# Optimization experiments

Measured on AMD Instinct MI355X. Metric: run time of the kernel, lower is better.

## Reference

```python
import jax, jax.numpy as jnp
from jax import lax
import numpy as np

D = 8        # domain_num
L = 12       # label_num
C = 9        # attr_num
W = 128      # window_size
B = 4096
EPS = 1e-5


def setup_inputs() -> dict:
    key = jax.random.key(0)
    ks = jax.random.split(key, 12)
    s = 0.05
    return {
        "x": jax.random.normal(ks[0], (B, C, 1, W), dtype=jnp.float32),
        "weights": jax.random.uniform(ks[1], (B, D), dtype=jnp.float32),
        # per-domain stacked parameters (leading dim D)
        "gamma": jnp.ones((D, C), dtype=jnp.float32),
        "beta": jnp.zeros((D, C), dtype=jnp.float32),
        "w1": jax.random.normal(ks[2], (D, 32, C, 9), dtype=jnp.float32) * s,
        "b1": jax.random.normal(ks[3], (D, 32), dtype=jnp.float32) * s,
        "w2": jax.random.normal(ks[4], (D, 64, 32, 9), dtype=jnp.float32) * s,
        "b2": jax.random.normal(ks[5], (D, 64), dtype=jnp.float32) * s,
        "fcw": jax.random.normal(ks[6], (D, L, 64 * 26), dtype=jnp.float32) * s,
        "fcb": jax.random.normal(ks[7], (D, L), dtype=jnp.float32) * s,
    }


def _maxpool2(h):
    # MaxPool along width, kernel 2 stride 2 (height is 1 and already squeezed)
    b, c, w = h.shape
    return h.reshape(b, c, w // 2, 2).max(axis=-1)


def _branch(x3, gamma, beta, w1, b1, w2, b2, fcw, fcb):
    # x3: [B, C, W]. BatchNorm2d in training mode: batch stats over (N, H, W).
    mean = x3.mean(axis=(0, 2), keepdims=True)
    var = x3.var(axis=(0, 2), keepdims=True)
    xn = (x3 - mean) * lax.rsqrt(var + EPS) * gamma[None, :, None] + beta[None, :, None]
    dn = ('NCH', 'OIH', 'NCH')
    h = lax.conv_general_dilated(xn, w1, (1,), 'VALID', dimension_numbers=dn)
    h = _maxpool2(jax.nn.relu(h + b1[None, :, None]))          # [B,32,60]
    h = lax.conv_general_dilated(h, w2, (1,), 'VALID', dimension_numbers=dn)
    h = _maxpool2(jax.nn.relu(h + b2[None, :, None]))          # [B,64,26]
    flat = h.reshape(h.shape[0], 64 * 26)
    return jax.nn.relu(flat @ fcw.T + fcb)                      # [B,L]


def reference(x, weights, gamma, beta, w1, b1, w2, b2, fcw, fcb):
    x3 = x[:, :, 0, :]  # squeeze height=1 -> [B,C,W]
    per_domain = jax.vmap(_branch, in_axes=(None, 0, 0, 0, 0, 0, 0, 0, 0))(
        x3, gamma, beta, w1, b1, w2, b2, fcw, fcb)              # [D,B,L]
    # vectorized form of the nested python-loop weighted sum over domains
    return jnp.einsum('bd,dbl->bl', weights, per_domain)        # [B,L]
```

## Files before the change

### kernel.cpp

```cpp
#include <hip/hip_runtime.h>
#include <hip/hip_bf16.h>

#define D 8
#define L 12
#define C 9
#define W 128
#define B 4096
#define EPS 1e-5f

typedef __attribute__((ext_vector_type(8))) short v8s;
typedef __attribute__((ext_vector_type(4))) float v4f;

#define OFF_STATS 0
#define OFF_B1E   18432
#define OFF_W1T   18688
#define OFF_W2T   39168
#define OFF_FCWP  112896

#define REGION 2336
#define STRIP  1152

__device__ inline unsigned short f2bf(float f) {
    unsigned u = __builtin_bit_cast(unsigned, f);
    u += 0x7FFFu + ((u >> 16) & 1u);
    return (unsigned short)(u >> 16);
}
__device__ inline unsigned pk2(float a, float b) {
    float2 f2; f2.x = a; f2.y = b;
    __hip_bfloat162 h = __float22bfloat162_rn(f2);
    unsigned u; __builtin_memcpy(&u, &h, 4);
    return u;
}

__global__ void stats_repack_kernel(const float* __restrict__ x,
                                    const float* __restrict__ w2,
                                    const float* __restrict__ fcw,
                                    float* __restrict__ ws,
                                    float* __restrict__ out) {
    const int t = threadIdx.x;
    __shared__ float red2[4][18];
    if (blockIdx.x < 1024) {
        const int rb = blockIdx.x * 4;
        const int w = t & 127, half = t >> 7;
        float s[9], s2[9];
        #pragma unroll
        for (int c = 0; c < 9; c++) { s[c] = 0.f; s2[c] = 0.f; }
        #pragma unroll
        for (int pass = 0; pass < 2; pass++) {
            const int row = rb + pass * 2 + half;
            const float* xr = x + (size_t)row * 1152 + w;
            #pragma unroll
            for (int c = 0; c < 9; c++) {
                float v = xr[c * 128];
                s[c] += v; s2[c] += v * v;
            }
        }
        #pragma unroll
        for (int c = 0; c < 9; c++) {
            #pragma unroll
            for (int off = 32; off >= 1; off >>= 1) {
                s[c]  += __shfl_down(s[c], off);
                s2[c] += __shfl_down(s2[c], off);
            }
        }
        if ((t & 63) == 0) {
            #pragma unroll
            for (int c = 0; c < 9; c++) {
                red2[t >> 6][c] = s[c]; red2[t >> 6][9 + c] = s2[c];
            }
        }
        __syncthreads();
        if (t < 18)
            ws[OFF_STATS + t * 1024 + blockIdx.x] =
                red2[0][t] + red2[1][t] + red2[2][t] + red2[3][t];
    } else if (blockIdx.x < 1152) {
        const int g = (blockIdx.x - 1024) * 4 + (t >> 6);
        const int lane = t & 63;
        const int d = g >> 6, o = g & 63;
        const float* src = w2 + (size_t)(d * 64 + o) * 288;
        short* dst = (short*)(ws + OFF_W2T) + (size_t)d * 18432 + o * 288;
        for (int i = lane; i < 288; i += 64) {
            int ic = i / 9, tap = i % 9;
            dst[tap * 32 + ic] = (short)f2bf(src[i]);
        }
    } else if (blockIdx.x < 1200) {
        const int g = (blockIdx.x - 1152) * 4 + (t >> 6);
        const int lane = t & 63;
        const int dl = g >> 1, half = g & 1;
        const float* src = fcw + (size_t)dl * 1664;
        short* dst = (short*)(ws + OFF_FCWP) + (size_t)dl * 1664;
        for (int i = half * 832 + lane; i < half * 832 + 832; i += 64) {
            int o = i / 26, p = i % 26;
            dst[p * 64 + o] = (short)f2bf(src[i]);
        }
    } else {
        const int base = (blockIdx.x - 1200) * 6144;
        float4 z; z.x = z.y = z.z = z.w = 0.f;
        float4* o4 = (float4*)(out + base);
        for (int i = t; i < 1536; i += 256) o4[i] = z;
    }
}

__global__ void fold1_kernel(const float* __restrict__ w1, const float* __restrict__ b1,
                             const float* __restrict__ gamma, const float* __restrict__ beta,
                             float* __restrict__ ws) {
    const int d = blockIdx.x, t = threadIdx.x;
    const int lane = t & 63, wvq = t >> 6;
    __shared__ float g[9], bt[9];
    for (int c = wvq; c < 9; c += 4) {
        float s = 0.f, s2 = 0.f;
        #pragma unroll
        for (int j = 0; j < 16; j++) {
            s  += ws[OFF_STATS + c * 1024 + lane + 64 * j];
            s2 += ws[OFF_STATS + (9 + c) * 1024 + lane + 64 * j];
        }
        #pragma unroll
        for (int off = 32; off >= 1; off >>= 1) {
            s  += __shfl_down(s, off);
            s2 += __shfl_down(s2, off);
        }
        if (lane == 0) {
            const float N = (float)B * (float)W;
            float m  = s / N;
            float vv = s2 / N - m * m;
            float inv = rsqrtf(vv + EPS);
            float gg = gamma[d * 9 + c] * inv;
            g[c] = gg; bt[c] = beta[d * 9 + c] - gg * m;
        }
    }
    __syncthreads();
    const int o = t >> 3, sub = t & 7;
    short* w1t = (short*)(ws + OFF_W1T);
    short* dst = w1t + (size_t)d * 3072 + o * 96;
    const float* src = w1 + ((size_t)(d * 32 + o)) * 81;
    for (int k = sub * 12; k < sub * 12 + 12; k++) {
        int tap, ch;
        if (k < 64)      { tap = (k >> 5) * 4 + ((k >> 3) & 3); ch = k & 7; }
        else {
            int q = (k >> 3) & 3, j = k & 7;
            if (q == 0)              { tap = 8; ch = j; }
            else if (q == 2)         { tap = j; ch = 8; }
            else if (q == 3 && j==0) { tap = 8; ch = 8; }
            else                     { tap = -1; ch = 0; }
        }
        float v = (tap >= 0) ? src[ch * 9 + tap] * g[ch] : 0.f;
        dst[k] = (short)f2bf(v);
    }
    float bias_part = 0.f;
    for (int tap = sub; tap < 9; tap += 8) {
        for (int c = 0; c < 9; c++)
            bias_part += src[c * 9 + tap] * bt[c];
    }
    bias_part += __shfl_xor(bias_part, 1);
    bias_part += __shfl_xor(bias_part, 2);
    bias_part += __shfl_xor(bias_part, 4);
    if (sub == 0) ws[OFF_B1E + d * 32 + o] = b1[d * 32 + o] + bias_part;
}

__global__ __launch_bounds__(256, 4)
void branch_kernel(const float* __restrict__ x,
                   const float* __restrict__ b2g,
                   const float* __restrict__ fcb,
                   const float* __restrict__ wts,
                   const float* __restrict__ ws,
                   float* __restrict__ out) {
    const int t = threadIdx.x;
    const int lane = t & 63;
    const int wv = t >> 6;
    const int d = blockIdx.y;
    const int b0 = blockIdx.x * 4;
    const short* w1t  = (const short*)(ws + OFF_W1T) + (size_t)d * 3072;
    const short* w2t  = (const short*)(ws + OFF_W2T) + (size_t)d * 18432;
    const short* fcwp = (const short*)(ws + OFF_FCWP) + (size_t)d * 12 * 1664;
    const float* b1e  = ws + OFF_B1E + d * 32;

    __shared__ __align__(16) short lds[4 * REGION];
    short* myr = &lds[wv * REGION];

    const int n = lane & 15, quad = lane >> 4;

    {
        const float* xrow = x + (size_t)(b0 + wv) * 1152;
        unsigned short c8s[2];
        #pragma unroll
        for (int rep = 0; rep < 2; rep++) {
            const int w = lane + rep * 64;
            float v[9];
            #pragma unroll
            for (int c = 0; c < 9; c++) v[c] = xrow[c * 128 + w];
            uint4 lo;
            lo.x = pk2(v[0], v[1]); lo.y = pk2(v[2], v[3]);
            lo.z = pk2(v[4], v[5]); lo.w = pk2(v[6], v[7]);
            *(uint4*)&myr[w * 8] = lo;
            c8s[rep] = f2bf(v[8]);
        }
        {
            uint4 z; z.x = z.y = z.z = z.w = 0;
            if (lane < 16) *(uint4*)&myr[(128 + lane) * 8] = z;
            if (lane < 24) *(uint4*)&myr[STRIP + (120 + lane) * 8] = z;
        }
        #pragma unroll
        for (int rep = 0; rep < 2; rep++) {
            const int w = lane + rep * 64;
            const short c8 = (short)c8s[rep];
            #pragma unroll
            for (int j = 0; j < 8; j++) {
                if (rep == 1 || lane >= j)
                    myr[STRIP + (w - j) * 8 + j] = c8;
            }
        }
    }

    {
        const float bias0 = b1e[n], bias1 = b1e[16 + n];
        v4f acc[8][2];
        #pragma unroll
        for (int mt = 0; mt < 8; mt++)
            #pragma unroll
            for (int nt = 0; nt < 2; nt++) { v4f z = {0.f,0.f,0.f,0.f}; acc[mt][nt] = z; }
        #pragma unroll
        for (int ck = 0; ck < 3; ck++) {
            v8s Bw0 = *(const v8s*)&w1t[n * 96 + ck * 32 + quad * 8];
            v8s Bw1 = *(const v8s*)&w1t[(16 + n) * 96 + ck * 32 + quad * 8];
            #pragma unroll
            for (int mt = 0; mt < 8; mt++) {
                const int rowm = mt * 16 + n;
                int aoff;
                if (ck < 2) aoff = (rowm + ck * 4 + quad) * 8;
                else        aoff = (quad < 2) ? (rowm + 8) * 8
                                              : (STRIP + (rowm + (quad - 2) * 8) * 8);
                v8s Af = *(const v8s*)&myr[aoff];
                acc[mt][0] = __builtin_amdgcn_mfma_f32_16x16x32_bf16(Af, Bw0, acc[mt][0], 0, 0, 0);
                acc[mt][1] = __builtin_amdgcn_mfma_f32_16x16x32_bf16(Af, Bw1, acc[mt][1], 0, 0, 0);
            }
        }
        unsigned held[16];
        #pragma unroll
        for (int mt = 0; mt < 8; mt++)
            #pragma unroll
            for (int nt = 0; nt < 2; nt++) {
                const float bb = nt ? bias1 : bias0;
                float h0  = fmaxf(fmaxf(acc[mt][nt][0], acc[mt][nt][1]) + bb, 0.f);
                float h1v = fmaxf(fmaxf(acc[mt][nt][2], acc[mt][nt][3]) + bb, 0.f);
                held[mt * 2 + nt] = pk2(h0, h1v);
            }
        #pragma unroll
        for (int mt = 0; mt < 8; mt++) {
            const int p = mt * 8 + quad * 2;
            #pragma unroll
            for (int nt = 0; nt < 2; nt++) {
                const unsigned pr = held[mt * 2 + nt];
                const int plane = nt * 2 + (n >> 3);
                const int col = n & 7;
                if (p < 60)     myr[(plane * 73 + p) * 8 + col]     = (short)(pr & 0xFFFFu);
                if (p + 1 < 60) myr[(plane * 73 + p + 1) * 8 + col] = (short)(pr >> 16);
            }
        }
    }

    {
        float biasv[4];
        #pragma unroll
        for (int nt = 0; nt < 4; nt++) biasv[nt] = b2g[d * 64 + nt * 16 + n];
        v4f acc[4][4];
        #pragma unroll
        for (int mt = 0; mt < 4; mt++)
            #pragma unroll
            for (int nt = 0; nt < 4; nt++) { v4f z = {0.f,0.f,0.f,0.f}; acc[mt][nt] = z; }
        for (int tap = 0; tap < 9; tap++) {
            v8s Bw[4];
            #pragma unroll
            for (int nt = 0; nt < 4; nt++)
                Bw[nt] = *(const v8s*)&w2t[(nt * 16 + n) * 288 + tap * 32 + quad * 8];
            #pragma unroll
            for (int mt = 0; mt < 4; mt++) {
                const int row = mt * 16 + n + tap;
                v8s Af = *(const v8s*)&myr[(quad * 73 + row) * 8];
                #pragma unroll
                for (int nt = 0; nt < 4; nt++)
                    acc[mt][nt] = __builtin_amdgcn_mfma_f32_16x16x32_bf16(Af, Bw[nt], acc[mt][nt], 0, 0, 0);
            }
        }
        unsigned held[16];
        #pragma unroll
        for (int mt = 0; mt < 4; mt++)
            #pragma unroll
            for (int nt = 0; nt < 4; nt++) {
                float h0  = fmaxf(fmaxf(acc[mt][nt][0], acc[mt][nt][1]) + biasv[nt], 0.f);
                float h1v = fmaxf(fmaxf(acc[mt][nt][2], acc[mt][nt][3]) + biasv[nt], 0.f);
                held[mt * 4 + nt] = pk2(h0, h1v);
            }
        #pragma unroll
        for (int mt = 0; mt < 4; mt++) {
            const int p = mt * 8 + quad * 2;
            #pragma unroll
            for (int nt = 0; nt < 4; nt++) {
                const unsigned pr = held[mt * 4 + nt];
                const int oc = nt * 16 + n;
                if (p < 26) {
                    const int gs = (oc >> 3) ^ (p & 7);
                    myr[p * 64 + gs * 8 + (oc & 7)] = (short)(pr & 0xFFFFu);
                }
                if (p + 1 < 26) {
                    const int gs = (oc >> 3) ^ ((p + 1) & 7);
                    myr[(p + 1) * 64 + gs * 8 + (oc & 7)] = (short)(pr >> 16);
                }
            }
        }
    }
    __syncthreads();

    {
        const int lrow = (n < 12) ? n : 0;
        v4f acc = {0.f, 0.f, 0.f, 0.f};
        for (int ks = wv; ks < 52; ks += 4) {
            const int p = ks >> 1;
            const int gs = ((ks & 1) * 4 + quad) ^ (p & 7);
            v8s A  = *(const v8s*)&fcwp[lrow * 1664 + ks * 32 + quad * 8];
            v8s Bf = *(const v8s*)&lds[(n & 3) * REGION + p * 64 + gs * 8];
            acc = __builtin_amdgcn_mfma_f32_16x16x32_bf16(A, Bf, acc, 0, 0, 0);
        }
        float* red = (float*)(myr + 1672);
        *(float4*)&red[lane * 4] = *(float4*)&acc;
    }
    __syncthreads();
    if (t < 64) {
        float sum[4] = {0.f, 0.f, 0.f, 0.f};
        #pragma unroll
        for (int w = 0; w < 4; w++) {
            const float* redw = (const float*)(&lds[w * REGION + 1672]);
            float4 v = *(const float4*)&redw[lane * 4];
            sum[0] += v.x; sum[1] += v.y; sum[2] += v.z; sum[3] += v.w;
        }
        if (n < 4) {
            const float wgt = wts[(size_t)(b0 + n) * 8 + d];
            #pragma unroll
            for (int r = 0; r < 4; r++) {
                const int l = quad * 4 + r;
                if (l < 12) {
                    float v = fmaxf(sum[r] + fcb[d * 12 + l], 0.f);
                    atomicAdd(&out[(size_t)(b0 + n) * 12 + l], wgt * v);
                }
            }
        }
    }
}

extern "C" void kernel_launch(void* const* d_in, const int* in_sizes, int n_in,
                              void* d_out, int out_size, void* d_ws, size_t ws_size,
                              hipStream_t stream) {
    const float* x       = (const float*)d_in[0];
    const float* weights = (const float*)d_in[1];
    const float* gamma   = (const float*)d_in[2];
    const float* beta    = (const float*)d_in[3];
    const float* w1      = (const float*)d_in[4];
    const float* b1      = (const float*)d_in[5];
    const float* w2      = (const float*)d_in[6];
    const float* b2      = (const float*)d_in[7];
    const float* fcw     = (const float*)d_in[8];
    const float* fcb     = (const float*)d_in[9];
    float* ws  = (float*)d_ws;
    float* out = (float*)d_out;

    stats_repack_kernel<<<dim3(1208), 256, 0, stream>>>(x, w2, fcw, ws, out);
    fold1_kernel<<<dim3(D), 256, 0, stream>>>(w1, b1, gamma, beta, ws);
    branch_kernel<<<dim3(B / 4, D), 256, 0, stream>>>(x, b2, fcb, weights, ws, out);
}
```

Before: 223.0 us.

## Fold BN weight folding into stats kernel via last-block atomic; shuffle-build channel-8 strip

Removes the separate fold1 kernel launch. The last stats block, identified by an atomic counter reset with a memset, reduces the statistics and writes the folded conv1 weights and bias for all domains. It also replaces the scattered per-element LDS stores that build the shifted channel-8 strip with wave shuffles and two vectorized 16-byte stores per lane. The trade is an extra memset and a serialized tail in one block that loops over all eight domains, in exchange for one fewer kernel launch.

```diff
diff --git a/kernel.cpp b/kernel.cpp
--- a/kernel.cpp
+++ b/kernel.cpp
@@ -16,6 +16,7 @@
 #define OFF_W1T   18688
 #define OFF_W2T   39168
 #define OFF_FCWP  112896
+#define OFF_CTR   192768
 
 #define REGION 2336
 #define STRIP  1152
@@ -35,10 +36,16 @@
 __global__ void stats_repack_kernel(const float* __restrict__ x,
                                     const float* __restrict__ w2,
                                     const float* __restrict__ fcw,
+                                    const float* __restrict__ gamma,
+                                    const float* __restrict__ beta,
+                                    const float* __restrict__ w1,
+                                    const float* __restrict__ b1,
                                     float* __restrict__ ws,
                                     float* __restrict__ out) {
     const int t = threadIdx.x;
     __shared__ float red2[4][18];
+    __shared__ float gI[9], gM[9], gld[9], btd[9];
+    __shared__ int isLast;
     if (blockIdx.x < 1024) {
         const int rb = blockIdx.x * 4;
         const int w = t & 127, half = t >> 7;
@@ -73,6 +80,70 @@
         if (t < 18)
             ws[OFF_STATS + t * 1024 + blockIdx.x] =
                 red2[0][t] + red2[1][t] + red2[2][t] + red2[3][t];
+        __threadfence();
+        __syncthreads();
+        if (t == 0) {
+            int old = atomicAdd((int*)(ws + OFF_CTR), 1);
+            isLast = (old == 1023);
+        }
+        __syncthreads();
+        if (isLast) {
+            __threadfence();
+            const int lane = t & 63, wv = t >> 6;
+            for (int c = wv; c < 9; c += 4) {
+                float rs = 0.f, rs2 = 0.f;
+                #pragma unroll
+                for (int j = 0; j < 16; j++) {
+                    rs  += ws[OFF_STATS + c * 1024 + lane + 64 * j];
+                    rs2 += ws[OFF_STATS + (9 + c) * 1024 + lane + 64 * j];
+                }
+                #pragma unroll
+                for (int off = 32; off >= 1; off >>= 1) {
+                    rs  += __shfl_down(rs, off);
+                    rs2 += __shfl_down(rs2, off);
+                }
+                if (lane == 0) {
+                    const float N = (float)B * (float)W;
+                    float m  = rs / N;
+                    float vv = rs2 / N - m * m;
+                    gI[c] = rsqrtf(vv + EPS); gM[c] = m;
+                }
+            }
+            __syncthreads();
+            const int o = t >> 3, sub = t & 7;
+            for (int d = 0; d < 8; d++) {
+                if (t < 9) {
+                    float gg = gamma[d * 9 + t] * gI[t];
+                    gld[t] = gg; btd[t] = beta[d * 9 + t] - gg * gM[t];
+                }
+                __syncthreads();
+                short* dst = (short*)(ws + OFF_W1T) + (size_t)d * 3072 + o * 96;
+                const float* src = w1 + ((size_t)(d * 32 + o)) * 81;
+                for (int k = sub * 12; k < sub * 12 + 12; k++) {
+                    int tap, ch;
+                    if (k < 64)      { tap = (k >> 5) * 4 + ((k >> 3) & 3); ch = k & 7; }
+                    else {
+                        int q = (k >> 3) & 3, j = k & 7;
+                        if (q == 0)               { tap = 8; ch = j; }
+                        else if (q == 2)          { tap = j; ch = 8; }
+                        else if (q == 3 && j==0)  { tap = 8; ch = 8; }
+                        else                      { tap = -1; ch = 0; }
+                    }
+                    float v = (tap >= 0) ? src[ch * 9 + tap] * gld[ch] : 0.f;
+                    dst[k] = (short)f2bf(v);
+                }
+                float bias_part = 0.f;
+                for (int tap = sub; tap < 9; tap += 8) {
+                    for (int c2 = 0; c2 < 9; c2++)
+                        bias_part += src[c2 * 9 + tap] * btd[c2];
+                }
+                bias_part += __shfl_xor(bias_part, 1);
+                bias_part += __shfl_xor(bias_part, 2);
+                bias_part += __shfl_xor(bias_part, 4);
+                if (sub == 0) ws[OFF_B1E + d * 32 + o] = b1[d * 32 + o] + bias_part;
+                __syncthreads();
+            }
+        }
     } else if (blockIdx.x < 1152) {
         const int g = (blockIdx.x - 1024) * 4 + (t >> 6);
         const int lane = t & 63;
@@ -99,62 +170,6 @@
         float4* o4 = (float4*)(out + base);
         for (int i = t; i < 1536; i += 256) o4[i] = z;
     }
-}
-
-__global__ void fold1_kernel(const float* __restrict__ w1, const float* __restrict__ b1,
-                             const float* __restrict__ gamma, const float* __restrict__ beta,
-                             float* __restrict__ ws) {
-    const int d = blockIdx.x, t = threadIdx.x;
-    const int lane = t & 63, wvq = t >> 6;
-    __shared__ float g[9], bt[9];
-    for (int c = wvq; c < 9; c += 4) {
-        float s = 0.f, s2 = 0.f;
-        #pragma unroll
-        for (int j = 0; j < 16; j++) {
-            s  += ws[OFF_STATS + c * 1024 + lane + 64 * j];
-            s2 += ws[OFF_STATS + (9 + c) * 1024 + lane + 64 * j];
-        }
-        #pragma unroll
-        for (int off = 32; off >= 1; off >>= 1) {
-            s  += __shfl_down(s, off);
-            s2 += __shfl_down(s2, off);
-        }
-        if (lane == 0) {
-            const float N = (float)B * (float)W;
-            float m  = s / N;
-            float vv = s2 / N - m * m;
-            float inv = rsqrtf(vv + EPS);
-            float gg = gamma[d * 9 + c] * inv;
-            g[c] = gg; bt[c] = beta[d * 9 + c] - gg * m;
-        }
-    }
-    __syncthreads();
-    const int o = t >> 3, sub = t & 7;
-    short* w1t = (short*)(ws + OFF_W1T);
-    short* dst = w1t + (size_t)d * 3072 + o * 96;
-    const float* src = w1 + ((size_t)(d * 32 + o)) * 81;
-    for (int k = sub * 12; k < sub * 12 + 12; k++) {
-        int tap, ch;
-        if (k < 64)      { tap = (k >> 5) * 4 + ((k >> 3) & 3); ch = k & 7; }
-        else {
-            int q = (k >> 3) & 3, j = k & 7;
-            if (q == 0)              { tap = 8; ch = j; }
-            else if (q == 2)         { tap = j; ch = 8; }
-            else if (q == 3 && j==0) { tap = 8; ch = 8; }
-            else                     { tap = -1; ch = 0; }
-        }
-        float v = (tap >= 0) ? src[ch * 9 + tap] * g[ch] : 0.f;
-        dst[k] = (short)f2bf(v);
-    }
-    float bias_part = 0.f;
-    for (int tap = sub; tap < 9; tap += 8) {
-        for (int c = 0; c < 9; c++)
-            bias_part += src[c * 9 + tap] * bt[c];
-    }
-    bias_part += __shfl_xor(bias_part, 1);
-    bias_part += __shfl_xor(bias_part, 2);
-    bias_part += __shfl_xor(bias_part, 4);
-    if (sub == 0) ws[OFF_B1E + d * 32 + o] = b1[d * 32 + o] + bias_part;
 }
 
 __global__ __launch_bounds__(256, 4)
@@ -181,7 +196,7 @@
 
     {
         const float* xrow = x + (size_t)(b0 + wv) * 1152;
-        unsigned short c8s[2];
+        int c8a = 0, c8b = 0;
         #pragma unroll
         for (int rep = 0; rep < 2; rep++) {
             const int w = lane + rep * 64;
@@ -192,23 +207,34 @@
             lo.x = pk2(v[0], v[1]); lo.y = pk2(v[2], v[3]);
             lo.z = pk2(v[4], v[5]); lo.w = pk2(v[6], v[7]);
             *(uint4*)&myr[w * 8] = lo;
-            c8s[rep] = f2bf(v[8]);
-        }
-        {
+            if (rep == 0) c8a = (int)f2bf(v[8]); else c8b = (int)f2bf(v[8]);
+        }
+        if (lane < 16) {
             uint4 z; z.x = z.y = z.z = z.w = 0;
-            if (lane < 16) *(uint4*)&myr[(128 + lane) * 8] = z;
-            if (lane < 24) *(uint4*)&myr[STRIP + (120 + lane) * 8] = z;
-        }
-        #pragma unroll
-        for (int rep = 0; rep < 2; rep++) {
-            const int w = lane + rep * 64;
-            const short c8 = (short)c8s[rep];
-            #pragma unroll
-            for (int j = 0; j < 8; j++) {
-                if (rep == 1 || lane >= j)
-                    myr[STRIP + (w - j) * 8 + j] = c8;
-            }
-        }
+            *(uint4*)&myr[(128 + lane) * 8] = z;
+            *(uint4*)&myr[STRIP + (128 + lane) * 8] = z;
+        }
+        unsigned short r0[8], r1[8];
+        r0[0] = (unsigned short)c8a; r1[0] = (unsigned short)c8b;
+        #pragma unroll
+        for (int j = 1; j < 8; j++) {
+            int s0 = __shfl(c8a, (lane + j) & 63);
+            int s1 = __shfl(c8b, (lane + j) & 63);
+            const bool in0 = (lane + j) < 64;
+            r0[j] = (unsigned short)(in0 ? s0 : s1);
+            r1[j] = (unsigned short)(in0 ? s1 : 0);
+        }
+        uint4 q0, q1;
+        q0.x = (unsigned)r0[0] | ((unsigned)r0[1] << 16);
+        q0.y = (unsigned)r0[2] | ((unsigned)r0[3] << 16);
+        q0.z = (unsigned)r0[4] | ((unsigned)r0[5] << 16);
+        q0.w = (unsigned)r0[6] | ((unsigned)r0[7] << 16);
+        q1.x = (unsigned)r1[0] | ((unsigned)r1[1] << 16);
+        q1.y = (unsigned)r1[2] | ((unsigned)r1[3] << 16);
+        q1.z = (unsigned)r1[4] | ((unsigned)r1[5] << 16);
+        q1.w = (unsigned)r1[6] | ((unsigned)r1[7] << 16);
+        *(uint4*)&myr[STRIP + lane * 8] = q0;
+        *(uint4*)&myr[STRIP + (64 + lane) * 8] = q1;
     }
 
     {
@@ -362,7 +388,8 @@
     float* ws  = (float*)d_ws;
     float* out = (float*)d_out;
 
-    stats_repack_kernel<<<dim3(1208), 256, 0, stream>>>(x, w2, fcw, ws, out);
-    fold1_kernel<<<dim3(D), 256, 0, stream>>>(w1, b1, gamma, beta, ws);
+    hipMemsetAsync(ws + OFF_CTR, 0, 4, stream);
+    stats_repack_kernel<<<dim3(1208), 256, 0, stream>>>(x, w2, fcw, gamma, beta,
+                                                        w1, b1, ws, out);
     branch_kernel<<<dim3(B / 4, D), 256, 0, stream>>>(x, b2, fcb, weights, ws, out);
 }
```

Result: slower. 336.1 us (+50.7%).
